# Kernel tuning notes

Measured on AMD Instinct MI355X. Metric: run time of the kernel, lower is better.

The kernel has to match this reference:

```python
import jax, jax.numpy as jnp
import numpy as np

N_NODES = 50000
N_EDGES = 600000
N_PAIRS = 200000
D_IN, D_HID = 128, 256


def _sage_conv(x, src, dst, W_l, b_l, W_r, num_nodes):
    # PyG SAGEConv('mean'): out = mean_agg(x_j) @ W_l + b_l + x @ W_r
    msgs = x[src]                                              # [E, d] gather
    agg = jax.ops.segment_sum(msgs, dst, num_segments=num_nodes)
    deg = jax.ops.segment_sum(jnp.ones((src.shape[0],), x.dtype), dst,
                              num_segments=num_nodes)
    agg = agg / jnp.maximum(deg, 1.0)[:, None]                 # mean, safe for deg=0
    return agg @ W_l + b_l + x @ W_r


def setup_inputs() -> dict:
    key = jax.random.key(0)
    ks = jax.random.split(key, 8)
    s = lambda d: 1.0 / np.sqrt(d)
    return {
        "features": jax.random.normal(ks[0], (N_NODES, D_IN), jnp.float32),
        "edge_index": jax.random.randint(ks[1], (2, N_EDGES), 0, N_NODES, jnp.int64),
        "mask": jax.random.randint(ks[2], (N_PAIRS, 2), 0, N_NODES, jnp.int64),
        "W1l": jax.random.normal(ks[3], (D_IN, D_HID), jnp.float32) * s(D_IN),
        "b1l": jnp.zeros((D_HID,), jnp.float32),
        "W1r": jax.random.normal(ks[4], (D_IN, D_HID), jnp.float32) * s(D_IN),
        "W2l": jax.random.normal(ks[5], (D_HID, D_IN), jnp.float32) * s(D_HID),
        "b2l": jnp.zeros((D_IN,), jnp.float32),
        "W2r": jax.random.normal(ks[6], (D_HID, D_IN), jnp.float32) * s(D_HID),
        "Wlin": jax.random.normal(ks[7], (2 * D_IN, 1), jnp.float32) * s(2 * D_IN),
        "blin": jnp.zeros((1,), jnp.float32),
    }


def reference(features, edge_index, mask, W1l, b1l, W1r, W2l, b2l, W2r, Wlin, blin):
    n = features.shape[0]
    src, dst = edge_index[0], edge_index[1]
    h = _sage_conv(features, src, dst, W1l, b1l, W1r, n)       # [N, 256]
    h = jax.nn.relu(h)                                         # dropout p=0 -> identity
    h = _sage_conv(h, src, dst, W2l, b2l, W2r, n)              # [N, 128]
    m = mask.T                                                 # [2, P]
    p1 = jax.lax.stop_gradient(h[m[0]])                        # detach in original
    p2 = jax.lax.stop_gradient(h[m[1]])
    pair = jnp.concatenate((p1, p2), axis=1)                   # [P, 256]
    return jax.nn.sigmoid(pair @ Wlin + blin)                  # [P, 1]
```

## Files before the change

### kernel.cpp

```cpp
#include <hip/hip_runtime.h>
#include <math.h>

#define NN 50000
#define NE 600000
#define NP 200000
#define NB_SCAN 49

typedef unsigned int uint;
typedef unsigned short ushort;
typedef __attribute__((ext_vector_type(8))) short bf16x8;
typedef __attribute__((ext_vector_type(4))) float f32x4;

__device__ __forceinline__ ushort f2bf(float f) {
    uint u = __float_as_uint(f);
    uint r = (u + 0x7FFFu + ((u >> 16) & 1u)) >> 16;
    return (ushort)r;
}
__device__ __forceinline__ float bf2f(uint lo16) {
    return __uint_as_float(lo16 << 16);
}

__device__ __forceinline__ int wave_iscan(int v, int lane) {
#pragma unroll
    for (int off = 1; off < 64; off <<= 1) {
        int t = __shfl_up(v, off, 64);
        if (lane >= off) v += t;
    }
    return v;
}

template <int K, int N>
__device__ __forceinline__ void prepB_one(int idx, const float* __restrict__ Wt,
                                          const float* __restrict__ Wb,
                                          ushort* __restrict__ Bp) {
    int lane = idx & 63;
    int nt = (idx >> 6) % (N / 16);
    int ct = idx / (64 * (N / 16));
    int n = nt * 16 + (lane & 15);
    int kb = ct * 32 + (lane >> 4) * 8;
#pragma unroll
    for (int j = 0; j < 8; j++) {
        int k = kb + j;
        float w = (k < K / 2) ? Wt[(size_t)k * N + n] : Wb[(size_t)(k - K / 2) * N + n];
        Bp[(size_t)idx * 8 + j] = f2bf(w);
    }
}

#define T_PREP (NN * 64)
#define T_DEG  (T_PREP + NE)
#define T_B1   (T_DEG + 8192)
#define T_PQ   (T_B1 + 1024)
#define T_CAB  (T_PQ + 2)
__global__ void k_pre(const float* __restrict__ x, uint* __restrict__ A1u,
                      const int* __restrict__ dst, int* __restrict__ deg,
                      const float* __restrict__ W1l, const float* __restrict__ W1r,
                      ushort* __restrict__ Bp1,
                      const float* __restrict__ W2l, const float* __restrict__ W2r,
                      const float* __restrict__ Wlin, const float* __restrict__ b2l,
                      float* __restrict__ pq, float* __restrict__ cab) {
    int t = blockIdx.x * 256 + threadIdx.x;
    if (t < T_PREP) {
        int n = t >> 6, c2 = t & 63;
        float2 v = *(const float2*)(x + (size_t)n * 128 + c2 * 2);
        A1u[(size_t)n * 128 + 64 + c2] = (uint)f2bf(v.x) | ((uint)f2bf(v.y) << 16);
    } else if (t < T_DEG) {
        atomicAdd(deg + dst[t - T_PREP], 1);
    } else if (t < T_B1) {
        prepB_one<256, 256>(t - T_DEG, W1l, W1r, Bp1);
    } else if (t < T_PQ) {
        int idx = t - T_B1;
        int vec = idx >> 8;
        int k = idx & 255;
        const float* W = (vec < 2) ? W2l : W2r;
        const float* wl = Wlin + (vec & 1) * 128;
        float s = 0.f;
#pragma unroll 4
        for (int j = 0; j < 128; j++) s += W[(size_t)k * 128 + j] * wl[j];
        pq[idx] = s;
    } else if (t < T_CAB) {
        int i = t - T_PQ;
        float s = 0.f;
        for (int j = 0; j < 128; j++) s += b2l[j] * Wlin[i * 128 + j];
        cab[i] = s;
    }
}

__global__ __launch_bounds__(1024) void k_scan1(const int* __restrict__ deg,
                                                int* __restrict__ excl,
                                                int* __restrict__ bsum) {
    int tid = threadIdx.x;
    int i = blockIdx.x * 1024 + tid;
    int lane = tid & 63, wid = tid >> 6;
    int v = (i < NN) ? deg[i] : 0;
    int incl = wave_iscan(v, lane);
    __shared__ int wt[16];
    if (lane == 63) wt[wid] = incl;
    __syncthreads();
    if (tid < 16) {
        int w = wt[tid];
#pragma unroll
        for (int off = 1; off < 16; off <<= 1) {
            int t = __shfl_up(w, off, 64);
            if (tid >= off) w += t;
        }
        wt[tid] = w;
    }
    __syncthreads();
    int base = (wid > 0) ? wt[wid - 1] : 0;
    if (i < NN) excl[i] = incl - v + base;
    if (tid == 0) bsum[blockIdx.x] = wt[15];
}

__global__ void k_scan2(int* __restrict__ bsum) {
    int lane = threadIdx.x;
    int v = (lane < NB_SCAN) ? bsum[lane] : 0;
    int incl = wave_iscan(v, lane);
    if (lane < NB_SCAN) bsum[lane] = incl - v;
}

__global__ __launch_bounds__(1024) void k_scan3(const int* __restrict__ excl,
                                                const int* __restrict__ bsum,
                                                int* __restrict__ rowptr,
                                                int* __restrict__ cursor) {
    int i = blockIdx.x * 1024 + threadIdx.x;
    if (i < NN) {
        int v = excl[i] + bsum[blockIdx.x];
        rowptr[i] = v;
        cursor[i] = v;
    }
    if (i == 0) rowptr[NN] = NE;
}

__global__ void k_fill(const int* __restrict__ src, const int* __restrict__ dst,
                       int* __restrict__ cursor, int* __restrict__ ssrc) {
    int e = blockIdx.x * 256 + threadIdx.x;
    if (e >= NE) return;
    int d = dst[e];
    int pos = atomicAdd(cursor + d, 1);
    ssrc[pos] = src[e];
}

__global__ void k_agg1(uint* __restrict__ A1u, const int* __restrict__ rowptr,
                       const int* __restrict__ ssrc) {
    int t = blockIdx.x * 256 + threadIdx.x;
    int n = t >> 6;
    if (n >= NN) return;
    int lane = t & 63;
    int r0 = rowptr[n], r1 = rowptr[n + 1];
    float ax0 = 0.f, ay0 = 0.f, ax1 = 0.f, ay1 = 0.f;
    float ax2 = 0.f, ay2 = 0.f, ax3 = 0.f, ay3 = 0.f;
    int e = r0;
    for (; e + 4 <= r1; e += 4) {
        int s0 = ssrc[e], s1 = ssrc[e + 1], s2 = ssrc[e + 2], s3 = ssrc[e + 3];
        uint v0 = A1u[(size_t)s0 * 128 + 64 + lane];
        uint v1 = A1u[(size_t)s1 * 128 + 64 + lane];
        uint v2 = A1u[(size_t)s2 * 128 + 64 + lane];
        uint v3 = A1u[(size_t)s3 * 128 + 64 + lane];
        ax0 += bf2f(v0 & 0xffffu); ay0 += bf2f(v0 >> 16);
        ax1 += bf2f(v1 & 0xffffu); ay1 += bf2f(v1 >> 16);
        ax2 += bf2f(v2 & 0xffffu); ay2 += bf2f(v2 >> 16);
        ax3 += bf2f(v3 & 0xffffu); ay3 += bf2f(v3 >> 16);
    }
    for (; e < r1; e++) {
        int s = ssrc[e];
        uint v = A1u[(size_t)s * 128 + 64 + lane];
        ax0 += bf2f(v & 0xffffu); ay0 += bf2f(v >> 16);
    }
    float ax = (ax0 + ax1) + (ax2 + ax3);
    float ay = (ay0 + ay1) + (ay2 + ay3);
    float sc = 1.0f / fmaxf((float)(r1 - r0), 1.0f);
    A1u[(size_t)n * 128 + lane] = (uint)f2bf(ax * sc) | ((uint)f2bf(ay * sc) << 16);
}

__global__ __launch_bounds__(256) void k_gemm1(const ushort* __restrict__ A,
                                               const ushort* __restrict__ Bp,
                                               const float* __restrict__ bias,
                                               const float* __restrict__ pq,
                                               float2* __restrict__ g2,
                                               float2* __restrict__ u2) {
    const int K = 256, NTW = 4;
    int wave = threadIdx.x >> 6;
    int lane = threadIdx.x & 63;
    int quad = lane >> 4;
    int l15 = lane & 15;
    int mbase = blockIdx.x * 32;
    int r0 = mbase + l15;       if (r0 >= NN) r0 = NN - 1;
    int r1 = mbase + 16 + l15;  if (r1 >= NN) r1 = NN - 1;
    f32x4 acc0[NTW], acc1[NTW];
#pragma unroll
    for (int i = 0; i < NTW; i++) {
        acc0[i] = (f32x4){0.f, 0.f, 0.f, 0.f};
        acc1[i] = (f32x4){0.f, 0.f, 0.f, 0.f};
    }
    const bf16x8* bp = (const bf16x8*)Bp;
#pragma unroll
    for (int ct = 0; ct < K / 32; ct++) {
        bf16x8 a0 = *(const bf16x8*)(A + (size_t)r0 * K + ct * 32 + quad * 8);
        bf16x8 a1 = *(const bf16x8*)(A + (size_t)r1 * K + ct * 32 + quad * 8);
#pragma unroll
        for (int ntl = 0; ntl < NTW; ntl++) {
            int nt = wave * NTW + ntl;
            bf16x8 b = bp[(ct * 16 + nt) * 64 + lane];
            acc0[ntl] = __builtin_amdgcn_mfma_f32_16x16x32_bf16(a0, b, acc0[ntl], 0, 0, 0);
            acc1[ntl] = __builtin_amdgcn_mfma_f32_16x16x32_bf16(a1, b, acc1[ntl], 0, 0, 0);
        }
    }
    float pga[2][4] = {{0,0,0,0},{0,0,0,0}}, pgb[2][4] = {{0,0,0,0},{0,0,0,0}};
    float pua[2][4] = {{0,0,0,0},{0,0,0,0}}, pub[2][4] = {{0,0,0,0},{0,0,0,0}};
#pragma unroll
    for (int ntl = 0; ntl < NTW; ntl++) {
        int col = (wave * NTW + ntl) * 16 + l15;
        float bv = bias[col];
        float wpa = pq[col], wpb = pq[256 + col];
        float wqa = pq[512 + col], wqb = pq[768 + col];
#pragma unroll
        for (int reg = 0; reg < 4; reg++) {
            float v0 = acc0[ntl][reg] + bv;  v0 = v0 > 0.f ? v0 : 0.f;
            float v1 = acc1[ntl][reg] + bv;  v1 = v1 > 0.f ? v1 : 0.f;
            pga[0][reg] += v0 * wpa;  pgb[0][reg] += v0 * wpb;
            pua[0][reg] += v0 * wqa;  pub[0][reg] += v0 * wqb;
            pga[1][reg] += v1 * wpa;  pgb[1][reg] += v1 * wpb;
            pua[1][reg] += v1 * wqa;  pub[1][reg] += v1 * wqb;
        }
    }
#pragma unroll
    for (int off = 1; off < 16; off <<= 1) {
#pragma unroll
        for (int rt = 0; rt < 2; rt++) {
#pragma unroll
            for (int reg = 0; reg < 4; reg++) {
                pga[rt][reg] += __shfl_xor(pga[rt][reg], off, 64);
                pgb[rt][reg] += __shfl_xor(pgb[rt][reg], off, 64);
                pua[rt][reg] += __shfl_xor(pua[rt][reg], off, 64);
                pub[rt][reg] += __shfl_xor(pub[rt][reg], off, 64);
            }
        }
    }
    __shared__ float red[4][4][32];
    if (l15 == 0) {
#pragma unroll
        for (int rt = 0; rt < 2; rt++) {
#pragma unroll
            for (int reg = 0; reg < 4; reg++) {
                int row = rt * 16 + quad * 4 + reg;
                red[0][wave][row] = pga[rt][reg];
                red[1][wave][row] = pgb[rt][reg];
                red[2][wave][row] = pua[rt][reg];
                red[3][wave][row] = pub[rt][reg];
            }
        }
    }
    __syncthreads();
    if (threadIdx.x < 32) {
        int row = threadIdx.x;
        int m = mbase + row;
        if (m < NN) {
            float ga = (red[0][0][row] + red[0][1][row]) + (red[0][2][row] + red[0][3][row]);
            float gb = (red[1][0][row] + red[1][1][row]) + (red[1][2][row] + red[1][3][row]);
            float ua = (red[2][0][row] + red[2][1][row]) + (red[2][2][row] + red[2][3][row]);
            float ub = (red[3][0][row] + red[3][1][row]) + (red[3][2][row] + red[3][3][row]);
            g2[m] = make_float2(ga, gb);
            u2[m] = make_float2(ua, ub);
        }
    }
}

__global__ void k_sagg(const float2* __restrict__ g2, const float2* __restrict__ u2,
                       const int* __restrict__ rowptr, const int* __restrict__ ssrc,
                       const float* __restrict__ cab,
                       float* __restrict__ sa, float* __restrict__ sb) {
    int n = blockIdx.x * 256 + threadIdx.x;
    if (n >= NN) return;
    int r0 = rowptr[n], r1 = rowptr[n + 1];
    float a0 = 0.f, b0 = 0.f, a1 = 0.f, b1 = 0.f;
    float a2 = 0.f, b2 = 0.f, a3 = 0.f, b3 = 0.f;
    int e = r0;
    for (; e + 4 <= r1; e += 4) {
        float2 v0 = g2[ssrc[e]];
        float2 v1 = g2[ssrc[e + 1]];
        float2 v2 = g2[ssrc[e + 2]];
        float2 v3 = g2[ssrc[e + 3]];
        a0 += v0.x; b0 += v0.y;
        a1 += v1.x; b1 += v1.y;
        a2 += v2.x; b2 += v2.y;
        a3 += v3.x; b3 += v3.y;
    }
    for (; e < r1; e++) {
        float2 v = g2[ssrc[e]];
        a0 += v.x; b0 += v.y;
    }
    float sc = 1.0f / fmaxf((float)(r1 - r0), 1.0f);
    float2 u = u2[n];
    sa[n] = ((a0 + a1) + (a2 + a3)) * sc + u.x + cab[0];
    sb[n] = ((b0 + b1) + (b2 + b3)) * sc + u.y + cab[1];
}

__global__ void k_pairs(const float* __restrict__ sa, const float* __restrict__ sb,
                        const int* __restrict__ mask, const float* __restrict__ blin,
                        float* __restrict__ out) {
    int p = blockIdx.x * 256 + threadIdx.x;
    if (p >= NP) return;
    int2 m = ((const int2*)mask)[p];
    float v = sa[m.x] + sb[m.y] + blin[0];
    out[p] = 1.0f / (1.0f + __expf(-v));
}

extern "C" void kernel_launch(void* const* d_in, const int* in_sizes, int n_in,
                              void* d_out, int out_size, void* d_ws, size_t ws_size,
                              hipStream_t stream) {
    const float* x    = (const float*)d_in[0];
    const int*   ei   = (const int*)  d_in[1];
    const int*   mask = (const int*)  d_in[2];
    const float* W1l  = (const float*)d_in[3];
    const float* b1l  = (const float*)d_in[4];
    const float* W1r  = (const float*)d_in[5];
    const float* W2l  = (const float*)d_in[6];
    const float* b2l  = (const float*)d_in[7];
    const float* W2r  = (const float*)d_in[8];
    const float* Wlin = (const float*)d_in[9];
    const float* blin = (const float*)d_in[10];
    float* out = (float*)d_out;

    const int* src = ei;
    const int* dst = ei + NE;

    char* ws = (char*)d_ws;
    int*    deg    = (int*)(ws);
    int*    rowptr = (int*)(ws + (size_t)1 * (1 << 20));
    int*    cursor = (int*)(ws + (size_t)2 * (1 << 20));
    int*    ssrc   = (int*)(ws + (size_t)3 * (1 << 20));
    int*    excl   = (int*)(ws + (size_t)6 * (1 << 20));
    int*    bsum   = (int*)(ws + (size_t)7 * (1 << 20));
    ushort* Bp1    = (ushort*)(ws + (size_t)8 * (1 << 20));
    float*  pq     = (float*)(ws + (size_t)9 * (1 << 20));
    float*  cab    = (float*)(ws + (size_t)9 * (1 << 20) + 65536);
    float*  sa     = (float*)(ws + (size_t)10 * (1 << 20));
    float*  sb     = (float*)(ws + (size_t)11 * (1 << 20));
    float2* g2     = (float2*)(ws + (size_t)12 * (1 << 20));
    float2* u2     = (float2*)(ws + (size_t)13 * (1 << 20));
    uint*   A1u    = (uint*)(ws + (size_t)14 * (1 << 20));

    hipMemsetAsync(deg, 0, (size_t)NN * 4, stream);

    k_pre  <<<(T_CAB + 255) / 256, 256, 0, stream>>>(x, A1u, dst, deg,
                                                     W1l, W1r, Bp1,
                                                     W2l, W2r, Wlin, b2l, pq, cab);
    k_scan1<<<NB_SCAN, 1024, 0, stream>>>(deg, excl, bsum);
    k_scan2<<<1, 64, 0, stream>>>(bsum);
    k_scan3<<<NB_SCAN, 1024, 0, stream>>>(excl, bsum, rowptr, cursor);
    k_fill <<<(NE + 255) / 256, 256, 0, stream>>>(src, dst, cursor, ssrc);

    k_agg1 <<<NN / 4, 256, 0, stream>>>(A1u, rowptr, ssrc);
    k_gemm1<<<(NN + 31) / 32, 256, 0, stream>>>((const ushort*)A1u, Bp1, b1l,
                                                pq, g2, u2);
    k_sagg <<<(NN + 255) / 256, 256, 0, stream>>>(g2, u2, rowptr, ssrc, cab, sa, sb);
    k_pairs<<<(NP + 255) / 256, 256, 0, stream>>>(sa, sb, mask, blin, out);
}
```

Baseline: 226.5 us.

## Fuse neighbor aggregation into GEMM1 via LDS and merge scan kernels

The layer-1 mean aggregation now runs inside the GEMM kernel. Each block aggregates its 32 nodes into shared memory and feeds the MFMA directly from LDS, so the aggregated rows are no longer written to and re-read from global memory. The bf16 feature copy shrinks to a compact 64-uint row layout with wider float4 conversion, and the two small scan kernels are merged into one, saving a launch. In exchange, aggregation parallelism drops: one block of 4 waves handles 32 nodes serially, 8 per wave, which may add latency on the gather.

```diff
diff --git a/kernel.cpp b/kernel.cpp
--- a/kernel.cpp
+++ b/kernel.cpp
@@ -46,12 +46,12 @@
     }
 }
 
-#define T_PREP (NN * 64)
+#define T_PREP (NN * 32)
 #define T_DEG  (T_PREP + NE)
 #define T_B1   (T_DEG + 8192)
 #define T_PQ   (T_B1 + 1024)
 #define T_CAB  (T_PQ + 2)
-__global__ void k_pre(const float* __restrict__ x, uint* __restrict__ A1u,
+__global__ void k_pre(const float* __restrict__ x, uint* __restrict__ xbf,
                       const int* __restrict__ dst, int* __restrict__ deg,
                       const float* __restrict__ W1l, const float* __restrict__ W1r,
                       ushort* __restrict__ Bp1,
@@ -60,9 +60,12 @@
                       float* __restrict__ pq, float* __restrict__ cab) {
     int t = blockIdx.x * 256 + threadIdx.x;
     if (t < T_PREP) {
-        int n = t >> 6, c2 = t & 63;
-        float2 v = *(const float2*)(x + (size_t)n * 128 + c2 * 2);
-        A1u[(size_t)n * 128 + 64 + c2] = (uint)f2bf(v.x) | ((uint)f2bf(v.y) << 16);
+        int n = t >> 5, c4 = t & 31;
+        float4 v = *(const float4*)(x + (size_t)n * 128 + c4 * 4);
+        uint2 o;
+        o.x = (uint)f2bf(v.x) | ((uint)f2bf(v.y) << 16);
+        o.y = (uint)f2bf(v.z) | ((uint)f2bf(v.w) << 16);
+        *(uint2*)(xbf + (size_t)n * 64 + c4 * 2) = o;
     } else if (t < T_DEG) {
         atomicAdd(deg + dst[t - T_PREP], 1);
     } else if (t < T_B1) {
@@ -111,20 +114,21 @@
     if (tid == 0) bsum[blockIdx.x] = wt[15];
 }
 
-__global__ void k_scan2(int* __restrict__ bsum) {
-    int lane = threadIdx.x;
-    int v = (lane < NB_SCAN) ? bsum[lane] : 0;
-    int incl = wave_iscan(v, lane);
-    if (lane < NB_SCAN) bsum[lane] = incl - v;
-}
-
-__global__ __launch_bounds__(1024) void k_scan3(const int* __restrict__ excl,
-                                                const int* __restrict__ bsum,
-                                                int* __restrict__ rowptr,
-                                                int* __restrict__ cursor) {
-    int i = blockIdx.x * 1024 + threadIdx.x;
+__global__ __launch_bounds__(1024) void k_scan23(const int* __restrict__ excl,
+                                                 const int* __restrict__ bsum,
+                                                 int* __restrict__ rowptr,
+                                                 int* __restrict__ cursor) {
+    __shared__ int boff;
+    int tid = threadIdx.x;
+    if (tid < 64) {
+        int v = (tid < NB_SCAN) ? bsum[tid] : 0;
+        int incl = wave_iscan(v, tid);
+        if (tid == (int)blockIdx.x) boff = incl - v;
+    }
+    __syncthreads();
+    int i = blockIdx.x * 1024 + tid;
     if (i < NN) {
-        int v = excl[i] + bsum[blockIdx.x];
+        int v = excl[i] + boff;
         rowptr[i] = v;
         cursor[i] = v;
     }
@@ -140,52 +144,53 @@
     ssrc[pos] = src[e];
 }
 
-__global__ void k_agg1(uint* __restrict__ A1u, const int* __restrict__ rowptr,
-                       const int* __restrict__ ssrc) {
-    int t = blockIdx.x * 256 + threadIdx.x;
-    int n = t >> 6;
-    if (n >= NN) return;
-    int lane = t & 63;
-    int r0 = rowptr[n], r1 = rowptr[n + 1];
-    float ax0 = 0.f, ay0 = 0.f, ax1 = 0.f, ay1 = 0.f;
-    float ax2 = 0.f, ay2 = 0.f, ax3 = 0.f, ay3 = 0.f;
-    int e = r0;
-    for (; e + 4 <= r1; e += 4) {
-        int s0 = ssrc[e], s1 = ssrc[e + 1], s2 = ssrc[e + 2], s3 = ssrc[e + 3];
-        uint v0 = A1u[(size_t)s0 * 128 + 64 + lane];
-        uint v1 = A1u[(size_t)s1 * 128 + 64 + lane];
-        uint v2 = A1u[(size_t)s2 * 128 + 64 + lane];
-        uint v3 = A1u[(size_t)s3 * 128 + 64 + lane];
-        ax0 += bf2f(v0 & 0xffffu); ay0 += bf2f(v0 >> 16);
-        ax1 += bf2f(v1 & 0xffffu); ay1 += bf2f(v1 >> 16);
-        ax2 += bf2f(v2 & 0xffffu); ay2 += bf2f(v2 >> 16);
-        ax3 += bf2f(v3 & 0xffffu); ay3 += bf2f(v3 >> 16);
-    }
-    for (; e < r1; e++) {
-        int s = ssrc[e];
-        uint v = A1u[(size_t)s * 128 + 64 + lane];
-        ax0 += bf2f(v & 0xffffu); ay0 += bf2f(v >> 16);
-    }
-    float ax = (ax0 + ax1) + (ax2 + ax3);
-    float ay = (ay0 + ay1) + (ay2 + ay3);
-    float sc = 1.0f / fmaxf((float)(r1 - r0), 1.0f);
-    A1u[(size_t)n * 128 + lane] = (uint)f2bf(ax * sc) | ((uint)f2bf(ay * sc) << 16);
-}
-
-__global__ __launch_bounds__(256) void k_gemm1(const ushort* __restrict__ A,
-                                               const ushort* __restrict__ Bp,
-                                               const float* __restrict__ bias,
-                                               const float* __restrict__ pq,
-                                               float2* __restrict__ g2,
-                                               float2* __restrict__ u2) {
-    const int K = 256, NTW = 4;
+__global__ __launch_bounds__(256) void k_gemm1f(const uint* __restrict__ xbf,
+                                                const int* __restrict__ rowptr,
+                                                const int* __restrict__ ssrc,
+                                                const ushort* __restrict__ Bp,
+                                                const float* __restrict__ bias,
+                                                const float* __restrict__ pq,
+                                                float2* __restrict__ g2,
+                                                float2* __restrict__ u2) {
+    const int NTW = 4;
+    __shared__ uint aggs[32][68];
+    __shared__ float red[4][4][32];
     int wave = threadIdx.x >> 6;
     int lane = threadIdx.x & 63;
     int quad = lane >> 4;
     int l15 = lane & 15;
     int mbase = blockIdx.x * 32;
-    int r0 = mbase + l15;       if (r0 >= NN) r0 = NN - 1;
-    int r1 = mbase + 16 + l15;  if (r1 >= NN) r1 = NN - 1;
+
+    for (int ln = wave * 8; ln < wave * 8 + 8; ln++) {
+        int m = mbase + ln;
+        int r0e = 0, r1e = 0;
+        if (m < NN) { r0e = rowptr[m]; r1e = rowptr[m + 1]; }
+        float ax0 = 0.f, ay0 = 0.f, ax1 = 0.f, ay1 = 0.f;
+        float ax2 = 0.f, ay2 = 0.f, ax3 = 0.f, ay3 = 0.f;
+        int e = r0e;
+        for (; e + 4 <= r1e; e += 4) {
+            uint v0 = xbf[(size_t)ssrc[e]     * 64 + lane];
+            uint v1 = xbf[(size_t)ssrc[e + 1] * 64 + lane];
+            uint v2 = xbf[(size_t)ssrc[e + 2] * 64 + lane];
+            uint v3 = xbf[(size_t)ssrc[e + 3] * 64 + lane];
+            ax0 += bf2f(v0 & 0xffffu); ay0 += bf2f(v0 >> 16);
+            ax1 += bf2f(v1 & 0xffffu); ay1 += bf2f(v1 >> 16);
+            ax2 += bf2f(v2 & 0xffffu); ay2 += bf2f(v2 >> 16);
+            ax3 += bf2f(v3 & 0xffffu); ay3 += bf2f(v3 >> 16);
+        }
+        for (; e < r1e; e++) {
+            uint v = xbf[(size_t)ssrc[e] * 64 + lane];
+            ax0 += bf2f(v & 0xffffu); ay0 += bf2f(v >> 16);
+        }
+        float ax = (ax0 + ax1) + (ax2 + ax3);
+        float ay = (ay0 + ay1) + (ay2 + ay3);
+        float sc = 1.0f / fmaxf((float)(r1e - r0e), 1.0f);
+        aggs[ln][lane] = (uint)f2bf(ax * sc) | ((uint)f2bf(ay * sc) << 16);
+    }
+    __syncthreads();
+
+    int r0g = mbase + l15;       if (r0g >= NN) r0g = NN - 1;
+    int r1g = mbase + 16 + l15;  if (r1g >= NN) r1g = NN - 1;
     f32x4 acc0[NTW], acc1[NTW];
 #pragma unroll
     for (int i = 0; i < NTW; i++) {
@@ -194,9 +199,9 @@
     }
     const bf16x8* bp = (const bf16x8*)Bp;
 #pragma unroll
-    for (int ct = 0; ct < K / 32; ct++) {
-        bf16x8 a0 = *(const bf16x8*)(A + (size_t)r0 * K + ct * 32 + quad * 8);
-        bf16x8 a1 = *(const bf16x8*)(A + (size_t)r1 * K + ct * 32 + quad * 8);
+    for (int ct = 0; ct < 4; ct++) {
+        bf16x8 a0 = *(const bf16x8*)&aggs[l15][ct * 16 + quad * 4];
+        bf16x8 a1 = *(const bf16x8*)&aggs[16 + l15][ct * 16 + quad * 4];
 #pragma unroll
         for (int ntl = 0; ntl < NTW; ntl++) {
             int nt = wave * NTW + ntl;
@@ -205,6 +210,20 @@
             acc1[ntl] = __builtin_amdgcn_mfma_f32_16x16x32_bf16(a1, b, acc1[ntl], 0, 0, 0);
         }
     }
+    const ushort* xb = (const ushort*)xbf;
+#pragma unroll
+    for (int ct = 4; ct < 8; ct++) {
+        bf16x8 a0 = *(const bf16x8*)(xb + (size_t)r0g * 128 + (ct - 4) * 32 + quad * 8);
+        bf16x8 a1 = *(const bf16x8*)(xb + (size_t)r1g * 128 + (ct - 4) * 32 + quad * 8);
+#pragma unroll
+        for (int ntl = 0; ntl < NTW; ntl++) {
+            int nt = wave * NTW + ntl;
+            bf16x8 b = bp[(ct * 16 + nt) * 64 + lane];
+            acc0[ntl] = __builtin_amdgcn_mfma_f32_16x16x32_bf16(a0, b, acc0[ntl], 0, 0, 0);
+            acc1[ntl] = __builtin_amdgcn_mfma_f32_16x16x32_bf16(a1, b, acc1[ntl], 0, 0, 0);
+        }
+    }
+
     float pga[2][4] = {{0,0,0,0},{0,0,0,0}}, pgb[2][4] = {{0,0,0,0},{0,0,0,0}};
     float pua[2][4] = {{0,0,0,0},{0,0,0,0}}, pub[2][4] = {{0,0,0,0},{0,0,0,0}};
 #pragma unroll
@@ -236,7 +255,6 @@
             }
         }
     }
-    __shared__ float red[4][4][32];
     if (l15 == 0) {
 #pragma unroll
         for (int rt = 0; rt < 2; rt++) {
@@ -338,21 +356,19 @@
     float*  sb     = (float*)(ws + (size_t)11 * (1 << 20));
     float2* g2     = (float2*)(ws + (size_t)12 * (1 << 20));
     float2* u2     = (float2*)(ws + (size_t)13 * (1 << 20));
-    uint*   A1u    = (uint*)(ws + (size_t)14 * (1 << 20));
+    uint*   xbf    = (uint*)(ws + (size_t)14 * (1 << 20));
 
     hipMemsetAsync(deg, 0, (size_t)NN * 4, stream);
 
-    k_pre  <<<(T_CAB + 255) / 256, 256, 0, stream>>>(x, A1u, dst, deg,
-                                                     W1l, W1r, Bp1,
-                                                     W2l, W2r, Wlin, b2l, pq, cab);
-    k_scan1<<<NB_SCAN, 1024, 0, stream>>>(deg, excl, bsum);
-    k_scan2<<<1, 64, 0, stream>>>(bsum);
-    k_scan3<<<NB_SCAN, 1024, 0, stream>>>(excl, bsum, rowptr, cursor);
-    k_fill <<<(NE + 255) / 256, 256, 0, stream>>>(src, dst, cursor, ssrc);
-
-    k_agg1 <<<NN / 4, 256, 0, stream>>>(A1u, rowptr, ssrc);
-    k_gemm1<<<(NN + 31) / 32, 256, 0, stream>>>((const ushort*)A1u, Bp1, b1l,
-                                                pq, g2, u2);
-    k_sagg <<<(NN + 255) / 256, 256, 0, stream>>>(g2, u2, rowptr, ssrc, cab, sa, sb);
-    k_pairs<<<(NP + 255) / 256, 256, 0, stream>>>(sa, sb, mask, blin, out);
-}
+    k_pre   <<<(T_CAB + 255) / 256, 256, 0, stream>>>(x, xbf, dst, deg,
+                                                      W1l, W1r, Bp1,
+                                                      W2l, W2r, Wlin, b2l, pq, cab);
+    k_scan1 <<<NB_SCAN, 1024, 0, stream>>>(deg, excl, bsum);
+    k_scan23<<<NB_SCAN, 1024, 0, stream>>>(excl, bsum, rowptr, cursor);
+    k_fill  <<<(NE + 255) / 256, 256, 0, stream>>>(src, dst, cursor, ssrc);
+
+    k_gemm1f<<<(NN + 31) / 32, 256, 0, stream>>>(xbf, rowptr, ssrc, Bp1, b1l,
+                                                 pq, g2, u2);
+    k_sagg  <<<(NN + 255) / 256, 256, 0, stream>>>(g2, u2, rowptr, ssrc, cab, sa, sb);
+    k_pairs <<<(NP + 255) / 256, 256, 0, stream>>>(sa, sb, mask, blin, out);
+}
```

Measured after the change: 256.1 us. +13.1%, slower.
